# Optimization experiments

Hardware: AMD Instinct MI355X
Metric: run time of the kernel (lower is better)

The kernel has to match this reference:

```python
import jax, jax.numpy as jnp
import numpy as np

IMG = 1536
STRIDES = [8, 16, 32, 64, 128]
SCALES = np.array([2.0 ** 0, 2.0 ** (1.0 / 3.0), 2.0 ** (2.0 / 3.0)])
RATIOS = np.array([0.5, 1.0, 2.0])
THRESHOLD = 0.5
IOU_THRESHOLD = 0.5
N_KEEP = 1000  # fixed candidate budget for jit-compatible NMS


def make_anchors():
    """Multi-level RetinaNet-style anchors in (x1, y1, x2, y2), [A, 4]."""
    all_boxes = []
    for s in STRIDES:
        base = 4.0 * s
        fs = IMG // s
        areas = (base * SCALES) ** 2
        ws, hs = [], []
        for r in RATIOS:
            ws.append(np.sqrt(areas / r))
            hs.append(np.sqrt(areas * r))
        ws = np.concatenate(ws)  # [9]
        hs = np.concatenate(hs)
        cx = (np.arange(fs) + 0.5) * s
        cy = (np.arange(fs) + 0.5) * s
        cxg, cyg = np.meshgrid(cx, cy)
        cxg = cxg.reshape(-1, 1)
        cyg = cyg.reshape(-1, 1)
        boxes = np.stack([cxg - ws / 2, cyg - hs / 2, cxg + ws / 2, cyg + hs / 2], axis=-1)
        all_boxes.append(boxes.reshape(-1, 4))
    return np.concatenate(all_boxes, axis=0).astype(np.float32)


def setup_inputs() -> dict:
    key = jax.random.key(0)
    k1, k2 = jax.random.split(key)
    anchors = jnp.asarray(make_anchors())  # [441936, 4]
    A = anchors.shape[0]
    cla = jax.random.uniform(k1, (1, A, 80), dtype=jnp.float32)  # sigmoid-like class scores
    reg = 0.1 * jax.random.normal(k2, (1, A, 4), dtype=jnp.float32)  # box deltas
    return {"cla": cla, "reg": reg, "anchors": anchors, "height": IMG, "width": IMG}


def decode_box(anchors, deltas):
    wa = anchors[:, 2] - anchors[:, 0]
    ha = anchors[:, 3] - anchors[:, 1]
    cxa = anchors[:, 0] + 0.5 * wa
    cya = anchors[:, 1] + 0.5 * ha
    cx = cxa + deltas[:, 0] * wa
    cy = cya + deltas[:, 1] * ha
    w = wa * jnp.exp(deltas[:, 2])
    h = ha * jnp.exp(deltas[:, 3])
    return jnp.stack([cx - 0.5 * w, cy - 0.5 * h, cx + 0.5 * w, cy + 0.5 * h], axis=-1)


def iou_matrix(b):
    x1 = jnp.maximum(b[:, None, 0], b[None, :, 0])
    y1 = jnp.maximum(b[:, None, 1], b[None, :, 1])
    x2 = jnp.minimum(b[:, None, 2], b[None, :, 2])
    y2 = jnp.minimum(b[:, None, 3], b[None, :, 3])
    inter = jnp.clip(x2 - x1, 0.0) * jnp.clip(y2 - y1, 0.0)
    area = jnp.clip(b[:, 2] - b[:, 0], 0.0) * jnp.clip(b[:, 3] - b[:, 1], 0.0)
    union = area[:, None] + area[None, :] - inter
    return inter / jnp.maximum(union, 1e-8)


def reference(cla, reg, anchors, height, width):
    # decode + clip (clipbox)
    boxes = decode_box(anchors, reg[0])  # [A, 4]
    boxes = jnp.stack([
        jnp.clip(boxes[:, 0], 0.0, width - 1.0),
        jnp.clip(boxes[:, 1], 0.0, height - 1.0),
        jnp.clip(boxes[:, 2], 0.0, width - 1.0),
        jnp.clip(boxes[:, 3], 0.0, height - 1.0),
    ], axis=-1)
    # per-anchor best class score (torch.max over dim=2)
    scores_all = jnp.max(cla[0], axis=1)  # [A]
    # fixed-size candidate set replaces data-dependent boolean masking
    top_scores, idx = jax.lax.top_k(scores_all, N_KEEP)
    cand_boxes = boxes[idx]            # [N, 4]
    cand_cla = cla[0][idx]             # [N, C]
    valid = top_scores > THRESHOLD     # score thresholding
    iou = iou_matrix(cand_boxes)       # [N, N]

    def body(i, keep):
        suppressed = jnp.any(keep & (iou[i] > IOU_THRESHOLD))
        return keep.at[i].set(valid[i] & ~suppressed)

    keep = jax.lax.fori_loop(0, N_KEEP, body, jnp.zeros((N_KEEP,), dtype=bool))

    nms_scores = jnp.where(keep, jnp.max(cand_cla, axis=1), 0.0)
    nms_class = jnp.where(keep, jnp.argmax(cand_cla, axis=1), -1)
    nms_boxes = jnp.where(keep[:, None], cand_boxes, 0.0)
    return nms_scores, nms_class, nms_boxes
```

## Files before the change

kernel.cpp:

```cpp
#include <hip/hip_runtime.h>
#include <stdint.h>


#define NK 1000
#define CAP 2048
#define NCLS 80
#define NW 16
typedef unsigned long long ull;

static inline __device__ unsigned fkey(float f) {
  unsigned u = __float_as_uint(f);
  return (u & 0x80000000u) ? ~u : (u | 0x80000000u);
}
static inline __device__ float fkey_inv(unsigned k) {
  unsigned u = (k & 0x80000000u) ? (k & 0x7fffffffu) : ~k;
  return __uint_as_float(u);
}

__device__ __forceinline__ void scan_select(const unsigned* __restrict__ gh, int nbins,
                                            unsigned k, unsigned* s_sum, unsigned* s_res,
                                            unsigned& digit, unsigned& cum_above) {
  int t = threadIdx.x;
  int chunk = nbins >> 8;
  int base = t * chunk;
  unsigned s = 0;
  for (int b = 0; b < chunk; ++b) s += gh[base + b];
  s_sum[t] = s;
  __syncthreads();
  unsigned ca = 0;
  for (int u = t + 1; u < 256; ++u) ca += s_sum[u];
  if (ca < k && ca + s >= k) {
    unsigned cum = ca;
    for (int b = chunk - 1; b >= 0; --b) {
      unsigned c = gh[base + b];
      if (cum + c >= k) { s_res[0] = (unsigned)(base + b); s_res[1] = cum; break; }
      cum += c;
    }
  }
  __syncthreads();
  digit = s_res[0];
  cum_above = s_res[1];
  __syncthreads();
}

__global__ __launch_bounds__(256) void k_score(const float* __restrict__ cla,
                                               unsigned* __restrict__ keys,
                                               unsigned* __restrict__ hist0, int A) {
  __shared__ unsigned lh[4096];
  int t = threadIdx.x;
  for (int i = t; i < 4096; i += 256) lh[i] = 0u;
  __syncthreads();
  const int lane = t & 63, wib = t >> 6;
  const int gwave = blockIdx.x * 4 + wib, nwaves = gridDim.x * 4;
  const int q = lane >> 2, sub = lane & 3;
  const int ntask = (A + 15) >> 4;
  for (int task = gwave; task < ntask; task += nwaves) {
    int a = task * 16 + q;
    float m = -3.402823466e38f;
    if (a < A) {
      const float4* p = (const float4*)(cla + (size_t)a * NCLS);
#pragma unroll
      for (int j = 0; j < 5; ++j) {
        float4 v = p[sub + j * 4];
        m = fmaxf(m, fmaxf(fmaxf(v.x, v.y), fmaxf(v.z, v.w)));
      }
    }
    m = fmaxf(m, __shfl_xor(m, 1, 64));
    m = fmaxf(m, __shfl_xor(m, 2, 64));
    if (sub == 0 && a < A) {
      unsigned key = fkey(m);
      keys[a] = key;
      atomicAdd(&lh[key >> 20], 1u);
    }
  }
  __syncthreads();
  for (int i = t; i < 4096; i += 256) {
    unsigned c = lh[i];
    if (c) atomicAdd(&hist0[i], c);
  }
}

__global__ __launch_bounds__(256) void k_hist1(const unsigned* __restrict__ keys,
                                               const unsigned* __restrict__ hist0,
                                               unsigned* __restrict__ hist1, int A) {
  __shared__ unsigned lh[4096];
  __shared__ unsigned s_sum[256];
  __shared__ unsigned s_res[2];
  int t = threadIdx.x;
  unsigned d0, ca;
  scan_select(hist0, 4096, NK, s_sum, s_res, d0, ca);
  for (int i = t; i < 4096; i += 256) lh[i] = 0u;
  __syncthreads();
  int tid = blockIdx.x * 256 + t, nthr = gridDim.x * 256;
  for (int a = tid; a < A; a += nthr) {
    unsigned key = keys[a];
    if ((key >> 20) == d0) atomicAdd(&lh[(key >> 8) & 0xFFFu], 1u);
  }
  __syncthreads();
  for (int i = t; i < 4096; i += 256) {
    unsigned c = lh[i];
    if (c) atomicAdd(&hist1[i], c);
  }
}

__global__ __launch_bounds__(256) void k_hist2(const unsigned* __restrict__ keys,
                                               const unsigned* __restrict__ hist0,
                                               const unsigned* __restrict__ hist1,
                                               unsigned* __restrict__ hist2, int A) {
  __shared__ unsigned lh[256];
  __shared__ unsigned s_sum[256];
  __shared__ unsigned s_res[2];
  int t = threadIdx.x;
  unsigned k_rem = NK, d0, d1, ca;
  scan_select(hist0, 4096, k_rem, s_sum, s_res, d0, ca);
  k_rem -= ca;
  scan_select(hist1, 4096, k_rem, s_sum, s_res, d1, ca);
  unsigned pref24 = (d0 << 12) | d1;
  lh[t] = 0u;
  __syncthreads();
  int tid = blockIdx.x * 256 + t, nthr = gridDim.x * 256;
  for (int a = tid; a < A; a += nthr) {
    unsigned key = keys[a];
    if ((key >> 8) == pref24) atomicAdd(&lh[key & 0xFFu], 1u);
  }
  __syncthreads();
  unsigned c = lh[t];
  if (c) atomicAdd(&hist2[t], c);
}

__global__ __launch_bounds__(256) void k_gather(const unsigned* __restrict__ keys,
                                                const unsigned* __restrict__ hist0,
                                                const unsigned* __restrict__ hist1,
                                                const unsigned* __restrict__ hist2,
                                                unsigned* __restrict__ cand_count,
                                                ull* __restrict__ cand_keys, int A) {
  __shared__ unsigned s_sum[256];
  __shared__ unsigned s_res[2];
  __shared__ ull lbuf[1024];
  __shared__ unsigned lcnt;
  __shared__ unsigned gbase;
  int t = threadIdx.x;
  unsigned k_rem = NK, d0, d1, d2, ca;
  scan_select(hist0, 4096, k_rem, s_sum, s_res, d0, ca);
  k_rem -= ca;
  scan_select(hist1, 4096, k_rem, s_sum, s_res, d1, ca);
  k_rem -= ca;
  scan_select(hist2, 256, k_rem, s_sum, s_res, d2, ca);
  const unsigned T = (((d0 << 12) | d1) << 8) | d2;
  if (t == 0) lcnt = 0u;
  __syncthreads();
  int tid = blockIdx.x * 256 + t, nthr = gridDim.x * 256;
  for (int a = tid; a < A; a += nthr) {
    unsigned key = keys[a];
    if (key >= T) {
      unsigned pos = atomicAdd(&lcnt, 1u);
      if (pos < 1024)
        lbuf[pos] = ((ull)key << 32) | (ull)(~(unsigned)a);
    }
  }
  __syncthreads();
  if (t == 0) gbase = (lcnt > 0) ? atomicAdd(cand_count, lcnt) : 0u;
  __syncthreads();
  unsigned n = lcnt < 1024u ? lcnt : 1024u;
  for (unsigned i = t; i < n; i += 256) {
    unsigned pos = gbase + i;
    if (pos < CAP) cand_keys[pos] = lbuf[i];
  }
}

__global__ __launch_bounds__(256) void k_rankdec(
    const float* __restrict__ cla, const float* __restrict__ reg,
    const float* __restrict__ anchors, const int* __restrict__ hp,
    const int* __restrict__ wp, const ull* __restrict__ cand_keys,
    float4* __restrict__ cand_box, float* __restrict__ cand_area,
    float* __restrict__ cand_score, int* __restrict__ cand_cls,
    int* __restrict__ cand_valid) {
  __shared__ ull skeys[CAP];
  int t = threadIdx.x;
  for (int i = t; i < CAP; i += 256) skeys[i] = cand_keys[i];
  __syncthreads();
  int c = blockIdx.x * 256 + t;
  ull ck = skeys[c];
  if (ck == 0ull) return;
  unsigned cnt = 0;
  const ulonglong2* sk2 = (const ulonglong2*)skeys;
#pragma unroll 4
  for (int j = 0; j < CAP / 2; ++j) {
    ulonglong2 v = sk2[j];
    cnt += (v.x > ck) ? 1u : 0u;
    cnt += (v.y > ck) ? 1u : 0u;
  }
  if (cnt >= NK) return;
  int rank = (int)cnt;
  unsigned a = ~(unsigned)(ck & 0xFFFFFFFFull);
  float score = fkey_inv((unsigned)(ck >> 32));
  float W1 = (float)wp[0] - 1.0f;
  float H1 = (float)hp[0] - 1.0f;
  float4 dd = ((const float4*)reg)[a];
  float4 an = ((const float4*)anchors)[a];
  float wa = an.z - an.x, ha = an.w - an.y;
  float cxa = an.x + 0.5f * wa, cya = an.y + 0.5f * ha;
  float cx = cxa + dd.x * wa, cy = cya + dd.y * ha;
  float w = wa * expf(dd.z), h = ha * expf(dd.w);
  float x1 = fminf(fmaxf(cx - 0.5f * w, 0.0f), W1);
  float y1 = fminf(fmaxf(cy - 0.5f * h, 0.0f), H1);
  float x2 = fminf(fmaxf(cx + 0.5f * w, 0.0f), W1);
  float y2 = fminf(fmaxf(cy + 0.5f * h, 0.0f), H1);
  cand_box[rank] = make_float4(x1, y1, x2, y2);
  cand_area[rank] = fmaxf(x2 - x1, 0.0f) * fmaxf(y2 - y1, 0.0f);
  cand_score[rank] = score;
  cand_valid[rank] = (score > 0.5f) ? 1 : 0;
  const float* row = cla + (size_t)a * NCLS;
  float m = -3.402823466e38f;
  int ci = 0;
#pragma unroll
  for (int j = 0; j < NCLS; ++j) {
    float v = row[j];
    if (v > m) { m = v; ci = j; }
  }
  cand_cls[rank] = ci;
}

__global__ __launch_bounds__(256) void k_supmat(const float4* __restrict__ cand_box,
                                                const float* __restrict__ cand_area,
                                                ull* __restrict__ sup) {
  __shared__ float4 bx[NK];
  __shared__ float ar[NK];
  int t = threadIdx.x;
  for (int i = t; i < NK; i += 256) {
    bx[i] = cand_box[i];
    ar[i] = cand_area[i];
  }
  __syncthreads();
  int g = blockIdx.x * 256 + t;
  int i = g >> 4, w = g & 15;
  if (i >= NK) return;
  float4 bi = bx[i];
  float ai = ar[i];
  ull bits = 0ull;
  int j0 = w * 64;
  int jend = (j0 + 64 < NK) ? (j0 + 64) : NK;
  for (int j = j0; j < jend; ++j) {
    float4 bj = bx[j];
    float xx1 = fmaxf(bi.x, bj.x), yy1 = fmaxf(bi.y, bj.y);
    float xx2 = fminf(bi.z, bj.z), yy2 = fminf(bi.w, bj.w);
    float inter = fmaxf(xx2 - xx1, 0.0f) * fmaxf(yy2 - yy1, 0.0f);
    float uni = ai + ar[j] - inter;
    float iou = inter / fmaxf(uni, 1e-8f);
    if (iou > 0.5f) bits |= (1ull << (j - j0));
  }
  sup[(size_t)i * NW + w] = bits;
}

__global__ __launch_bounds__(1024) void k_resolve(const ull* __restrict__ sup,
                                                  const int* __restrict__ cand_valid,
                                                  const float* __restrict__ cand_score,
                                                  const int* __restrict__ cand_cls,
                                                  const float4* __restrict__ cand_box,
                                                  float* __restrict__ out) {
  __shared__ ull keep_sh[NW];
  int t = threadIdx.x;
  if (t < 64) {
    int lane = t;
    ull keepw[NW];
#pragma unroll
    for (int c = 0; c < NW; ++c) {
      int row = c * 64 + lane;
      ull rw[NW];
      int vld = 0;
      if (row < NK) {
#pragma unroll
        for (int w = 0; w < NW; ++w) rw[w] = sup[(size_t)row * NW + w];
        vld = cand_valid[row];
      } else {
#pragma unroll
        for (int w = 0; w < NW; ++w) rw[w] = 0ull;
      }
      ull prev = 0ull;
#pragma unroll
      for (int w = 0; w < NW; ++w)
        if (w < c) prev |= rw[w] & keepw[w];
      int flags = (vld ? 2 : 0) | ((prev != 0ull) ? 1 : 0);
      unsigned Llo = (unsigned)rw[c];
      unsigned Lhi = (unsigned)(rw[c] >> 32);
      ull kept = 0ull;
      for (int b = 0; b < 64; ++b) {
        int fb = __shfl(flags, b, 64);
        unsigned lo = (unsigned)__shfl((int)Llo, b, 64);
        unsigned hi = (unsigned)__shfl((int)Lhi, b, 64);
        ull Lb = ((ull)hi << 32) | (ull)lo;
        bool kp = ((fb & 2) != 0) && ((fb & 1) == 0) && ((Lb & kept) == 0ull);
        kept |= ((ull)(kp ? 1u : 0u)) << b;
      }
      keepw[c] = kept;
    }
    if (lane == 0) {
#pragma unroll
      for (int w = 0; w < NW; ++w) keep_sh[w] = keepw[w];
    }
  }
  __syncthreads();
  for (int i = t; i < NK; i += 1024) {
    bool kp = (keep_sh[i >> 6] >> (i & 63)) & 1ull;
    out[i] = kp ? cand_score[i] : 0.0f;
    out[NK + i] = kp ? (float)cand_cls[i] : -1.0f;
    float4 b = cand_box[i];
    ((float4*)(out + 2 * NK))[i] = kp ? b : make_float4(0.f, 0.f, 0.f, 0.f);
  }
}

extern "C" void kernel_launch(void* const* d_in, const int* in_sizes, int n_in,
                              void* d_out, int out_size, void* d_ws, size_t ws_size,
                              hipStream_t stream) {
  const float* cla = (const float*)d_in[0];
  const float* reg = (const float*)d_in[1];
  const float* anchors = (const float*)d_in[2];
  const int* hp = (const int*)d_in[3];
  const int* wp = (const int*)d_in[4];
  float* out = (float*)d_out;
  int A = in_sizes[2] / 4;

  char* ws = (char*)d_ws;
  size_t off = 0;
  auto carve = [&](size_t bytes) -> void* {
    void* p = ws + off;
    off += bytes;
    off = (off + 255) & ~(size_t)255;
    return p;
  };
  unsigned* keys = (unsigned*)carve((size_t)A * 4);
  char* zbase = ws + off;
  unsigned* hist0 = (unsigned*)carve(4096 * 4);
  unsigned* hist1 = (unsigned*)carve(4096 * 4);
  unsigned* hist2 = (unsigned*)carve(256 * 4);
  unsigned* cand_count = (unsigned*)carve(4);
  ull* cand_keys = (ull*)carve(CAP * 8);
  size_t zbytes = (size_t)((ws + off) - zbase);
  float4* cand_box = (float4*)carve(1024 * 16);
  float* cand_area = (float*)carve(1024 * 4);
  float* cand_score = (float*)carve(1024 * 4);
  int* cand_cls = (int*)carve(1024 * 4);
  int* cand_valid = (int*)carve(1024 * 4);
  ull* sup = (ull*)carve((size_t)1024 * NW * 8);
  (void)ws_size;
  (void)n_in;
  (void)out_size;

  hipMemsetAsync(zbase, 0, zbytes, stream);
  k_score<<<1024, 256, 0, stream>>>(cla, keys, hist0, A);
  k_hist1<<<512, 256, 0, stream>>>(keys, hist0, hist1, A);
  k_hist2<<<512, 256, 0, stream>>>(keys, hist0, hist1, hist2, A);
  k_gather<<<512, 256, 0, stream>>>(keys, hist0, hist1, hist2, cand_count, cand_keys, A);
  k_rankdec<<<8, 256, 0, stream>>>(cla, reg, anchors, hp, wp, cand_keys, cand_box,
                                   cand_area, cand_score, cand_cls, cand_valid);
  k_supmat<<<63, 256, 0, stream>>>(cand_box, cand_area, sup);
  k_resolve<<<1, 1024, 0, stream>>>(sup, cand_valid, cand_score, cand_cls, cand_box, out);
}
```

Measured before the change: 356.3 us.

## Drop third radix pass, fuse rank/decode/IoU/resolve into one bitonic-sorted block

Removes the third histogram pass and gathers every key whose top 24 bits are at or above the selected prefix, with the candidate buffer raised to 4096. A single 1024-thread block then bitonic-sorts the candidates in LDS, decodes the top 1000, builds the suppression matrix and resolves NMS, replacing four separate launches. The NMS resolve switches from a 64-step shuffle loop to a ballot and ctz loop that visits only surviving candidates. This cuts launch count and full passes over the keys, but the suppression matrix, previously built across 63 blocks, now runs in one block, and the sort adds many barriers.

```diff
diff --git a/kernel.cpp b/kernel.cpp
--- a/kernel.cpp
+++ b/kernel.cpp
@@ -3,7 +3,7 @@
 
 
 #define NK 1000
-#define CAP 2048
+#define CAP 4096
 #define NCLS 80
 #define NW 16
 typedef unsigned long long ull;
@@ -20,21 +20,25 @@
 __device__ __forceinline__ void scan_select(const unsigned* __restrict__ gh, int nbins,
                                             unsigned k, unsigned* s_sum, unsigned* s_res,
                                             unsigned& digit, unsigned& cum_above) {
-  int t = threadIdx.x;
-  int chunk = nbins >> 8;
-  int base = t * chunk;
-  unsigned s = 0;
-  for (int b = 0; b < chunk; ++b) s += gh[base + b];
-  s_sum[t] = s;
-  __syncthreads();
-  unsigned ca = 0;
-  for (int u = t + 1; u < 256; ++u) ca += s_sum[u];
-  if (ca < k && ca + s >= k) {
-    unsigned cum = ca;
-    for (int b = chunk - 1; b >= 0; --b) {
-      unsigned c = gh[base + b];
-      if (cum + c >= k) { s_res[0] = (unsigned)(base + b); s_res[1] = cum; break; }
-      cum += c;
+  const int t = threadIdx.x;
+  const int chunk = nbins >> 8;
+  if (t < 256) {
+    unsigned s = 0;
+    for (int b = 0; b < chunk; ++b) s += gh[t * chunk + b];
+    s_sum[t] = s;
+  }
+  __syncthreads();
+  if (t < 256) {
+    unsigned ca = 0;
+    for (int u = t + 1; u < 256; ++u) ca += s_sum[u];
+    unsigned s = s_sum[t];
+    if (ca < k && ca + s >= k) {
+      unsigned cum = ca;
+      for (int b = chunk - 1; b >= 0; --b) {
+        unsigned c = gh[t * chunk + b];
+        if (cum + c >= k) { s_res[0] = (unsigned)(t * chunk + b); s_res[1] = cum; break; }
+        cum += c;
+      }
     }
   }
   __syncthreads();
@@ -103,175 +107,144 @@
   }
 }
 
-__global__ __launch_bounds__(256) void k_hist2(const unsigned* __restrict__ keys,
-                                               const unsigned* __restrict__ hist0,
-                                               const unsigned* __restrict__ hist1,
-                                               unsigned* __restrict__ hist2, int A) {
-  __shared__ unsigned lh[256];
+__global__ __launch_bounds__(256) void k_gather2(const unsigned* __restrict__ keys,
+                                                 const unsigned* __restrict__ hist0,
+                                                 const unsigned* __restrict__ hist1,
+                                                 unsigned* __restrict__ cand_count,
+                                                 ull* __restrict__ cand_keys, int A) {
   __shared__ unsigned s_sum[256];
   __shared__ unsigned s_res[2];
+  __shared__ ull lbuf[1024];
+  __shared__ unsigned lcnt, gbase;
   int t = threadIdx.x;
   unsigned k_rem = NK, d0, d1, ca;
   scan_select(hist0, 4096, k_rem, s_sum, s_res, d0, ca);
   k_rem -= ca;
   scan_select(hist1, 4096, k_rem, s_sum, s_res, d1, ca);
-  unsigned pref24 = (d0 << 12) | d1;
-  lh[t] = 0u;
+  const unsigned prefix24 = (d0 << 12) | d1;
+  if (t == 0) lcnt = 0u;
   __syncthreads();
   int tid = blockIdx.x * 256 + t, nthr = gridDim.x * 256;
   for (int a = tid; a < A; a += nthr) {
     unsigned key = keys[a];
-    if ((key >> 8) == pref24) atomicAdd(&lh[key & 0xFFu], 1u);
-  }
-  __syncthreads();
-  unsigned c = lh[t];
-  if (c) atomicAdd(&hist2[t], c);
-}
-
-__global__ __launch_bounds__(256) void k_gather(const unsigned* __restrict__ keys,
-                                                const unsigned* __restrict__ hist0,
-                                                const unsigned* __restrict__ hist1,
-                                                const unsigned* __restrict__ hist2,
-                                                unsigned* __restrict__ cand_count,
-                                                ull* __restrict__ cand_keys, int A) {
-  __shared__ unsigned s_sum[256];
-  __shared__ unsigned s_res[2];
-  __shared__ ull lbuf[1024];
-  __shared__ unsigned lcnt;
-  __shared__ unsigned gbase;
-  int t = threadIdx.x;
-  unsigned k_rem = NK, d0, d1, d2, ca;
-  scan_select(hist0, 4096, k_rem, s_sum, s_res, d0, ca);
-  k_rem -= ca;
-  scan_select(hist1, 4096, k_rem, s_sum, s_res, d1, ca);
-  k_rem -= ca;
-  scan_select(hist2, 256, k_rem, s_sum, s_res, d2, ca);
-  const unsigned T = (((d0 << 12) | d1) << 8) | d2;
-  if (t == 0) lcnt = 0u;
-  __syncthreads();
-  int tid = blockIdx.x * 256 + t, nthr = gridDim.x * 256;
-  for (int a = tid; a < A; a += nthr) {
-    unsigned key = keys[a];
-    if (key >= T) {
-      unsigned pos = atomicAdd(&lcnt, 1u);
-      if (pos < 1024)
-        lbuf[pos] = ((ull)key << 32) | (ull)(~(unsigned)a);
-    }
-  }
-  __syncthreads();
-  if (t == 0) gbase = (lcnt > 0) ? atomicAdd(cand_count, lcnt) : 0u;
+    if ((key >> 8) >= prefix24) {
+      unsigned p = atomicAdd(&lcnt, 1u);
+      if (p < 1024) lbuf[p] = ((ull)key << 32) | (ull)(~(unsigned)a);
+    }
+  }
+  __syncthreads();
+  if (t == 0) {
+    unsigned n = lcnt < 1024u ? lcnt : 1024u;
+    gbase = n ? atomicAdd(cand_count, n) : 0u;
+  }
   __syncthreads();
   unsigned n = lcnt < 1024u ? lcnt : 1024u;
   for (unsigned i = t; i < n; i += 256) {
-    unsigned pos = gbase + i;
-    if (pos < CAP) cand_keys[pos] = lbuf[i];
-  }
-}
-
-__global__ __launch_bounds__(256) void k_rankdec(
+    unsigned p = gbase + i;
+    if (p < CAP) cand_keys[p] = lbuf[i];
+  }
+}
+
+__global__ __launch_bounds__(1024) void k_final(
     const float* __restrict__ cla, const float* __restrict__ reg,
     const float* __restrict__ anchors, const int* __restrict__ hp,
     const int* __restrict__ wp, const ull* __restrict__ cand_keys,
-    float4* __restrict__ cand_box, float* __restrict__ cand_area,
-    float* __restrict__ cand_score, int* __restrict__ cand_cls,
-    int* __restrict__ cand_valid) {
-  __shared__ ull skeys[CAP];
-  int t = threadIdx.x;
-  for (int i = t; i < CAP; i += 256) skeys[i] = cand_keys[i];
-  __syncthreads();
-  int c = blockIdx.x * 256 + t;
-  ull ck = skeys[c];
-  if (ck == 0ull) return;
-  unsigned cnt = 0;
-  const ulonglong2* sk2 = (const ulonglong2*)skeys;
-#pragma unroll 4
-  for (int j = 0; j < CAP / 2; ++j) {
-    ulonglong2 v = sk2[j];
-    cnt += (v.x > ck) ? 1u : 0u;
-    cnt += (v.y > ck) ? 1u : 0u;
-  }
-  if (cnt >= NK) return;
-  int rank = (int)cnt;
-  unsigned a = ~(unsigned)(ck & 0xFFFFFFFFull);
-  float score = fkey_inv((unsigned)(ck >> 32));
-  float W1 = (float)wp[0] - 1.0f;
-  float H1 = (float)hp[0] - 1.0f;
-  float4 dd = ((const float4*)reg)[a];
-  float4 an = ((const float4*)anchors)[a];
-  float wa = an.z - an.x, ha = an.w - an.y;
-  float cxa = an.x + 0.5f * wa, cya = an.y + 0.5f * ha;
-  float cx = cxa + dd.x * wa, cy = cya + dd.y * ha;
-  float w = wa * expf(dd.z), h = ha * expf(dd.w);
-  float x1 = fminf(fmaxf(cx - 0.5f * w, 0.0f), W1);
-  float y1 = fminf(fmaxf(cy - 0.5f * h, 0.0f), H1);
-  float x2 = fminf(fmaxf(cx + 0.5f * w, 0.0f), W1);
-  float y2 = fminf(fmaxf(cy + 0.5f * h, 0.0f), H1);
-  cand_box[rank] = make_float4(x1, y1, x2, y2);
-  cand_area[rank] = fmaxf(x2 - x1, 0.0f) * fmaxf(y2 - y1, 0.0f);
-  cand_score[rank] = score;
-  cand_valid[rank] = (score > 0.5f) ? 1 : 0;
-  const float* row = cla + (size_t)a * NCLS;
-  float m = -3.402823466e38f;
-  int ci = 0;
-#pragma unroll
-  for (int j = 0; j < NCLS; ++j) {
-    float v = row[j];
-    if (v > m) { m = v; ci = j; }
-  }
-  cand_cls[rank] = ci;
-}
-
-__global__ __launch_bounds__(256) void k_supmat(const float4* __restrict__ cand_box,
-                                                const float* __restrict__ cand_area,
-                                                ull* __restrict__ sup) {
-  __shared__ float4 bx[NK];
-  __shared__ float ar[NK];
-  int t = threadIdx.x;
-  for (int i = t; i < NK; i += 256) {
-    bx[i] = cand_box[i];
-    ar[i] = cand_area[i];
-  }
-  __syncthreads();
-  int g = blockIdx.x * 256 + t;
-  int i = g >> 4, w = g & 15;
-  if (i >= NK) return;
-  float4 bi = bx[i];
-  float ai = ar[i];
-  ull bits = 0ull;
-  int j0 = w * 64;
-  int jend = (j0 + 64 < NK) ? (j0 + 64) : NK;
-  for (int j = j0; j < jend; ++j) {
-    float4 bj = bx[j];
-    float xx1 = fmaxf(bi.x, bj.x), yy1 = fmaxf(bi.y, bj.y);
-    float xx2 = fminf(bi.z, bj.z), yy2 = fminf(bi.w, bj.w);
-    float inter = fmaxf(xx2 - xx1, 0.0f) * fmaxf(yy2 - yy1, 0.0f);
-    float uni = ai + ar[j] - inter;
-    float iou = inter / fmaxf(uni, 1e-8f);
-    if (iou > 0.5f) bits |= (1ull << (j - j0));
-  }
-  sup[(size_t)i * NW + w] = bits;
-}
-
-__global__ __launch_bounds__(1024) void k_resolve(const ull* __restrict__ sup,
-                                                  const int* __restrict__ cand_valid,
-                                                  const float* __restrict__ cand_score,
-                                                  const int* __restrict__ cand_cls,
-                                                  const float4* __restrict__ cand_box,
-                                                  float* __restrict__ out) {
+    ull* __restrict__ sup, float* __restrict__ out) {
+  __shared__ __align__(16) ull bufC[CAP];
   __shared__ ull keep_sh[NW];
-  int t = threadIdx.x;
+  const int t = threadIdx.x;
+
+  for (int i = t; i < CAP; i += 1024) bufC[i] = cand_keys[i];
+  __syncthreads();
+
+  for (unsigned k2 = 2; k2 <= CAP; k2 <<= 1) {
+    for (unsigned j = k2 >> 1; j > 0; j >>= 1) {
+      for (int i = t; i < CAP; i += 1024) {
+        int ixj = i ^ (int)j;
+        if (ixj > i) {
+          ull x = bufC[i], y = bufC[ixj];
+          bool up = ((i & k2) == 0);
+          if (up ? (x < y) : (x > y)) { bufC[i] = y; bufC[ixj] = x; }
+        }
+      }
+      __syncthreads();
+    }
+  }
+
+  float4 boxr = make_float4(0.f, 0.f, 0.f, 0.f);
+  float arear = 0.f, scorer = 0.f;
+  int clsr = 0;
+  if (t < NK) {
+    ull ck = bufC[t];
+    unsigned a = ~(unsigned)(ck & 0xFFFFFFFFull);
+    scorer = fkey_inv((unsigned)(ck >> 32));
+    float W1 = (float)wp[0] - 1.0f;
+    float H1 = (float)hp[0] - 1.0f;
+    float4 dd = ((const float4*)reg)[a];
+    float4 an = ((const float4*)anchors)[a];
+    float wa = an.z - an.x, ha = an.w - an.y;
+    float cxa = an.x + 0.5f * wa, cya = an.y + 0.5f * ha;
+    float cx = cxa + dd.x * wa, cy = cya + dd.y * ha;
+    float w = wa * expf(dd.z), h = ha * expf(dd.w);
+    float x1 = fminf(fmaxf(cx - 0.5f * w, 0.0f), W1);
+    float y1 = fminf(fmaxf(cy - 0.5f * h, 0.0f), H1);
+    float x2 = fminf(fmaxf(cx + 0.5f * w, 0.0f), W1);
+    float y2 = fminf(fmaxf(cy + 0.5f * h, 0.0f), H1);
+    boxr = make_float4(x1, y1, x2, y2);
+    arear = fmaxf(x2 - x1, 0.0f) * fmaxf(y2 - y1, 0.0f);
+    const float* rowp = cla + (size_t)a * NCLS;
+    float m = -3.402823466e38f;
+#pragma unroll
+    for (int j = 0; j < NCLS; ++j) {
+      float v = rowp[j];
+      if (v > m) { m = v; clsr = j; }
+    }
+  }
+  __syncthreads();
+  float4* sbox = (float4*)bufC;
+  float* sarea = (float*)(bufC + 2048);
+  float* sscore = (float*)(bufC + 2560);
+  int* scls = (int*)(bufC + 3072);
+  if (t < 1024) {
+    sbox[t] = boxr;
+    sarea[t] = arear;
+    sscore[t] = scorer;
+    scls[t] = clsr;
+  }
+  __syncthreads();
+
+  for (int task = t; task < NK * NW; task += 1024) {
+    int i = task >> 4, w = task & 15;
+    float4 bi = sbox[i];
+    float ai = sarea[i];
+    ull bits = 0ull;
+    int j0 = w * 64;
+    int jend = (j0 + 64 < NK) ? (j0 + 64) : NK;
+    for (int j = j0; j < jend; ++j) {
+      float4 bj = sbox[j];
+      float xx1 = fmaxf(bi.x, bj.x), yy1 = fmaxf(bi.y, bj.y);
+      float xx2 = fminf(bi.z, bj.z), yy2 = fminf(bi.w, bj.w);
+      float inter = fmaxf(xx2 - xx1, 0.0f) * fmaxf(yy2 - yy1, 0.0f);
+      float uni = ai + sarea[j] - inter;
+      float iou = inter / fmaxf(uni, 1e-8f);
+      if (iou > 0.5f) bits |= (1ull << (j - j0));
+    }
+    sup[(size_t)i * NW + w] = bits;
+  }
+  __syncthreads();
+
   if (t < 64) {
-    int lane = t;
+    const int lane = t;
     ull keepw[NW];
 #pragma unroll
     for (int c = 0; c < NW; ++c) {
-      int row = c * 64 + lane;
+      const int row = c * 64 + lane;
       ull rw[NW];
       int vld = 0;
       if (row < NK) {
 #pragma unroll
         for (int w = 0; w < NW; ++w) rw[w] = sup[(size_t)row * NW + w];
-        vld = cand_valid[row];
+        vld = (sscore[row] > 0.5f) ? 1 : 0;
       } else {
 #pragma unroll
         for (int w = 0; w < NW; ++w) rw[w] = 0ull;
@@ -280,32 +253,31 @@
 #pragma unroll
       for (int w = 0; w < NW; ++w)
         if (w < c) prev |= rw[w] & keepw[w];
-      int flags = (vld ? 2 : 0) | ((prev != 0ull) ? 1 : 0);
-      unsigned Llo = (unsigned)rw[c];
-      unsigned Lhi = (unsigned)(rw[c] >> 32);
+      bool candf = vld && (prev == 0ull);
+      ull remaining = __ballot(candf);
+      ull Lc = rw[c];
       ull kept = 0ull;
-      for (int b = 0; b < 64; ++b) {
-        int fb = __shfl(flags, b, 64);
-        unsigned lo = (unsigned)__shfl((int)Llo, b, 64);
-        unsigned hi = (unsigned)__shfl((int)Lhi, b, 64);
-        ull Lb = ((ull)hi << 32) | (ull)lo;
-        bool kp = ((fb & 2) != 0) && ((fb & 1) == 0) && ((Lb & kept) == 0ull);
-        kept |= ((ull)(kp ? 1u : 0u)) << b;
+      while (remaining) {
+        int b = (int)__builtin_ctzll(remaining);
+        ull Lb = __shfl(Lc, b, 64);
+        kept |= (1ull << b);
+        remaining &= ~Lb;
+        remaining &= ~(1ull << b);
       }
       keepw[c] = kept;
     }
-    if (lane == 0) {
+    if (lane == 0)
 #pragma unroll
       for (int w = 0; w < NW; ++w) keep_sh[w] = keepw[w];
-    }
-  }
-  __syncthreads();
-  for (int i = t; i < NK; i += 1024) {
-    bool kp = (keep_sh[i >> 6] >> (i & 63)) & 1ull;
-    out[i] = kp ? cand_score[i] : 0.0f;
-    out[NK + i] = kp ? (float)cand_cls[i] : -1.0f;
-    float4 b = cand_box[i];
-    ((float4*)(out + 2 * NK))[i] = kp ? b : make_float4(0.f, 0.f, 0.f, 0.f);
+  }
+  __syncthreads();
+
+  if (t < NK) {
+    bool kp = (keep_sh[t >> 6] >> (t & 63)) & 1ull;
+    out[t] = kp ? sscore[t] : 0.0f;
+    out[NK + t] = kp ? (float)scls[t] : -1.0f;
+    float4 b = sbox[t];
+    ((float4*)(out + 2 * NK))[t] = kp ? b : make_float4(0.f, 0.f, 0.f, 0.f);
   }
 }
 
@@ -332,15 +304,9 @@
   char* zbase = ws + off;
   unsigned* hist0 = (unsigned*)carve(4096 * 4);
   unsigned* hist1 = (unsigned*)carve(4096 * 4);
-  unsigned* hist2 = (unsigned*)carve(256 * 4);
-  unsigned* cand_count = (unsigned*)carve(4);
-  ull* cand_keys = (ull*)carve(CAP * 8);
+  unsigned* cand_count = (unsigned*)carve(16 * 4);
+  ull* cand_keys = (ull*)carve((size_t)CAP * 8);
   size_t zbytes = (size_t)((ws + off) - zbase);
-  float4* cand_box = (float4*)carve(1024 * 16);
-  float* cand_area = (float*)carve(1024 * 4);
-  float* cand_score = (float*)carve(1024 * 4);
-  int* cand_cls = (int*)carve(1024 * 4);
-  int* cand_valid = (int*)carve(1024 * 4);
   ull* sup = (ull*)carve((size_t)1024 * NW * 8);
   (void)ws_size;
   (void)n_in;
@@ -349,10 +315,6 @@
   hipMemsetAsync(zbase, 0, zbytes, stream);
   k_score<<<1024, 256, 0, stream>>>(cla, keys, hist0, A);
   k_hist1<<<512, 256, 0, stream>>>(keys, hist0, hist1, A);
-  k_hist2<<<512, 256, 0, stream>>>(keys, hist0, hist1, hist2, A);
-  k_gather<<<512, 256, 0, stream>>>(keys, hist0, hist1, hist2, cand_count, cand_keys, A);
-  k_rankdec<<<8, 256, 0, stream>>>(cla, reg, anchors, hp, wp, cand_keys, cand_box,
-                                   cand_area, cand_score, cand_cls, cand_valid);
-  k_supmat<<<63, 256, 0, stream>>>(cand_box, cand_area, sup);
-  k_resolve<<<1, 1024, 0, stream>>>(sup, cand_valid, cand_score, cand_cls, cand_box, out);
-}
+  k_gather2<<<512, 256, 0, stream>>>(keys, hist0, hist1, cand_count, cand_keys, A);
+  k_final<<<1, 1024, 0, stream>>>(cla, reg, anchors, hp, wp, cand_keys, sup, out);
+}
```

Result: slower. 914.1 us (+156.5%).
